# Kernel tuning notes

Hardware: AMD Instinct MI355X
Metric: run time of the kernel (lower is better)

Reference implementation:

```python
import jax, jax.numpy as jnp
import numpy as np

B, S, DIM = 2, 2048, 2048
NH, NKV = 16, 16
HD = 128            # constructor head_dim (full per-head dim, = 2 * self.head_dim)
HHD = HD // 2       # self.head_dim = per-stream dim = 64
ROPE_THETA = 10000.0
LAMBDA_INIT = 0.8 - 0.6 * float(np.exp(-0.3 * 0))  # block_id = 0 -> 0.2
EPS = 1e-5


def make_freq_cis(seq_len, dim, theta):
    # rotation matrices, shape (seq, dim//2, 2, 2): [[cos, -sin], [sin, cos]]
    inv = 1.0 / (theta ** (np.arange(0, dim, 2, dtype=np.float32) / dim))
    ang = np.arange(seq_len, dtype=np.float32)[:, None] * inv[None, :]
    cos, sin = np.cos(ang), np.sin(ang)
    fc = np.stack([np.stack([cos, -sin], -1), np.stack([sin, cos], -1)], -2)
    return jnp.asarray(fc, dtype=jnp.float32)


def setup_inputs() -> dict:
    key = jax.random.key(0)
    ks = jax.random.split(key, 9)
    std = DIM ** -0.5
    return {
        "x": jax.random.normal(ks[0], (B, S, DIM), jnp.float32),
        "freq_cis": make_freq_cis(S, HD, ROPE_THETA),
        "wq": jax.random.normal(ks[1], (NH * HD, DIM), jnp.float32) * std,
        "wk": jax.random.normal(ks[2], (NKV * HD, DIM), jnp.float32) * std,
        "wv": jax.random.normal(ks[3], (NKV * HD, DIM), jnp.float32) * std,
        "wo": jax.random.normal(ks[4], (DIM, NH * HD), jnp.float32) * std,
        "lambda_q1": jax.random.normal(ks[5], (HHD,), jnp.float32) * 0.1,
        "lambda_k1": jax.random.normal(ks[6], (HHD,), jnp.float32) * 0.1,
        "lambda_q2": jax.random.normal(ks[7], (HHD,), jnp.float32) * 0.1,
        "lambda_k2": jax.random.normal(ks[8], (HHD,), jnp.float32) * 0.1,
        "subln_w": jnp.ones((HD,), jnp.float32),
    }


def _rope(t, fc):
    # t: (b, s, h, d); fc: (s, d//2, 2, 2). Pairs (even, odd) rotated by 2x2 matrix.
    b, s, h, d = t.shape
    t2 = t.reshape(b, s, h, d // 2, 1, 2)
    out = (t2 * fc[None, :, None]).sum(-1)  # (b, s, h, d//2, 2)
    return out.reshape(b, s, h, d)


def _causal_attn(q, k, v):
    # q, k: (b, s, h, HHD); v: (b, s, h, HD). Flash-attn default scale = 1/sqrt(q head dim).
    scale = 1.0 / jnp.sqrt(jnp.asarray(q.shape[-1], q.dtype))
    scores = jnp.einsum('bqhd,bkhd->bhqk', q, k) * scale
    s = q.shape[1]
    causal = jnp.tril(jnp.ones((s, s), bool))
    scores = jnp.where(causal, scores, jnp.finfo(scores.dtype).min)
    p = jax.nn.softmax(scores, axis=-1)
    return jnp.einsum('bhqk,bkhd->bqhd', p, v)  # (b, s, h, HD)


def reference(x, freq_cis, wq, wk, wv, wo, lambda_q1, lambda_k1, lambda_q2, lambda_k2, subln_w):
    b, s, _ = x.shape
    xq = (x @ wq.T).reshape(b, s, NH, HD)
    xk = (x @ wk.T).reshape(b, s, NKV, HD)
    xv = (x @ wv.T).reshape(b, s, NKV, HD)
    xq = _rope(xq, freq_cis)
    xk = _rope(xk, freq_cis)
    if NKV != NH:  # GQA: repeat kv heads group-wise
        rep = NH // NKV
        xk = jnp.repeat(xk, rep, axis=2)
        xv = jnp.repeat(xv, rep, axis=2)
    # split each head into two differential streams of size HHD
    xq = xq.reshape(b, s, NH, 2, HHD)
    xk = xk.reshape(b, s, NH, 2, HHD)
    attn1 = _causal_attn(xq[:, :, :, 0], xk[:, :, :, 0], xv)
    attn2 = _causal_attn(xq[:, :, :, 1], xk[:, :, :, 1], xv)
    lam1 = jnp.exp(jnp.sum(lambda_q1 * lambda_k1))
    lam2 = jnp.exp(jnp.sum(lambda_q2 * lambda_k2))
    lam_full = lam1 - lam2 + LAMBDA_INIT
    attn = attn1 - lam_full * attn2              # (b, s, h, HD)
    attn = jnp.transpose(attn, (0, 2, 1, 3))     # faithful to torch .transpose(1, 2)
    ms = jnp.mean(jnp.square(attn), axis=-1, keepdims=True)
    attn = attn * jax.lax.rsqrt(ms + EPS) * subln_w  # RMSNorm(2*HHD)
    attn = attn * (1.0 - LAMBDA_INIT)
    # faithful to original: reshape (b, h, s, HD) row-major into (b, s, h*HD)
    attn = attn.reshape(b, s, NH * HD)
    return attn @ wo.T
```

## Files before the change

### kernel.cpp

```cpp
#include <hip/hip_runtime.h>

typedef unsigned short u16;
typedef unsigned int   u32;
typedef __attribute__((ext_vector_type(8))) short s16x8;
typedef __attribute__((ext_vector_type(4))) float f32x4;

constexpr int Bc = 2, Sc = 2048, DIMc = 2048, NHc = 16, HDc = 128, Tc = Bc * Sc;
constexpr float LAMBDA_INIT_C = 0.2f;

__device__ __forceinline__ u16 f2bf(float f) {
  union { float f; u32 u; } v; v.f = f;
  u32 r = v.u + 0x7fffu + ((v.u >> 16) & 1u);
  return (u16)(r >> 16);
}
__device__ __forceinline__ float bf2f(u16 b) {
  union { u32 u; float f; } v; v.u = ((u32)b) << 16;
  return v.f;
}
__device__ __forceinline__ f32x4 mfma16(s16x8 a, s16x8 b, f32x4 c) {
  return __builtin_amdgcn_mfma_f32_16x16x32_bf16(a, b, c, 0, 0, 0);
}

typedef const __attribute__((address_space(1))) u32 gq32;
typedef __attribute__((address_space(3))) u32 lq32;
__device__ __forceinline__ void cp16(const u16* g, u16* l) {
  __builtin_amdgcn_global_load_lds((gq32*)g, (lq32*)l, 16, 0, 0);
}

__global__ void cvt_all_kernel(const float* __restrict__ x,
                               const float* __restrict__ wq, const float* __restrict__ wk,
                               const float* __restrict__ wv, const float* __restrict__ wo,
                               u16* __restrict__ xb, u16* __restrict__ wb) {
  const int i = blockIdx.x * 256 + threadIdx.x;
  constexpr int NX = Tc * DIMc / 4;
  constexpr int PW = DIMc * DIMc / 4;
  float4 v; uint2* dst;
  if (i < NX) {
    v = ((const float4*)x)[i];
    dst = ((uint2*)xb) + i;
  } else {
    const int j = i - NX;
    const int which = j >> 20;
    const int jj = j & (PW - 1);
    const float* src = which == 0 ? wq : which == 1 ? wk : which == 2 ? wv : wo;
    v = ((const float4*)src)[jj];
    dst = ((uint2*)wb) + j;
  }
  union { u16 u[4]; uint2 p; } o;
  o.u[0] = f2bf(v.x); o.u[1] = f2bf(v.y); o.u[2] = f2bf(v.z); o.u[3] = f2bf(v.w);
  *dst = o.p;
}

__global__ __launch_bounds__(256) void gemm_qkv(const u16* __restrict__ A,
                                                const u16* __restrict__ Wq,
                                                const u16* __restrict__ Wk,
                                                const u16* __restrict__ Wv,
                                                u16* __restrict__ Oq,
                                                u16* __restrict__ Ok,
                                                u16* __restrict__ Ov) {
  constexpr int K = DIMc, N = DIMc;
  __shared__ u16 lA[128 * 32];
  __shared__ u16 lB[128 * 32];
  const int nglob = blockIdx.x * 128;
  const int which = nglob >> 11;
  const u16* Bw = which == 0 ? Wq : which == 1 ? Wk : Wv;
  u16*       Cb = which == 0 ? Oq : which == 1 ? Ok : Ov;
  const int nbase = nglob & (N - 1);
  const int mbase = blockIdx.y * 128;

  const int tid  = threadIdx.x;
  const int lane = tid & 63;
  const int w    = tid >> 6;
  const int wrow = (w >> 1) * 64;
  const int wcol = (w & 1) * 64;
  const int l15  = lane & 15;
  const int quad = lane >> 4;

  f32x4 acc[4][4];
#pragma unroll
  for (int i = 0; i < 4; i++)
#pragma unroll
    for (int j = 0; j < 4; j++) acc[i][j] = (f32x4){0.f, 0.f, 0.f, 0.f};

  const int srow = w * 32 + (lane >> 2);
  const int scol = (lane & 3) * 8;
  const u16* gA = A  + (size_t)(mbase + srow) * K + scol;
  const u16* gB = Bw + (size_t)(nbase + srow) * K + scol;
  u16* sA = lA + srow * 32 + scol;
  u16* sB = lB + srow * 32 + scol;

  for (int kb = 0; kb < K; kb += 32) {
    __syncthreads();
    cp16(gA + kb,                  sA);
    cp16(gA + kb + (size_t)16 * K, sA + 16 * 32);
    cp16(gB + kb,                  sB);
    cp16(gB + kb + (size_t)16 * K, sB + 16 * 32);
    __syncthreads();
    s16x8 af[4], bfr[4];
#pragma unroll
    for (int i = 0; i < 4; i++)
      af[i] = *(const s16x8*)(lA + (wrow + i * 16 + l15) * 32 + quad * 8);
#pragma unroll
    for (int j = 0; j < 4; j++)
      bfr[j] = *(const s16x8*)(lB + (wcol + j * 16 + l15) * 32 + quad * 8);
#pragma unroll
    for (int i = 0; i < 4; i++)
#pragma unroll
      for (int j = 0; j < 4; j++) acc[i][j] = mfma16(af[i], bfr[j], acc[i][j]);
  }

#pragma unroll
  for (int i = 0; i < 4; i++) {
    const int m0 = mbase + wrow + i * 16 + quad * 4;
#pragma unroll
    for (int j = 0; j < 4; j++) {
      const int n0 = nbase + wcol + j * 16 + l15;
#pragma unroll
      for (int r = 0; r < 4; r++) Cb[(size_t)(m0 + r) * N + n0] = f2bf(acc[i][j][r]);
    }
  }
}

__global__ __launch_bounds__(256) void gemm_bt(const u16* __restrict__ A,
                                               const u16* __restrict__ Bw,
                                               float* __restrict__ Cf,
                                               int M, int N, int K) {
  __shared__ u16 lA[128 * 32];
  __shared__ u16 lB[128 * 32];
  const int tid  = threadIdx.x;
  const int lane = tid & 63;
  const int w    = tid >> 6;
  const int mbase = blockIdx.y * 128;
  const int nbase = blockIdx.x * 128;
  const int wrow = (w >> 1) * 64;
  const int wcol = (w & 1) * 64;
  const int l15  = lane & 15;
  const int quad = lane >> 4;

  f32x4 acc[4][4];
#pragma unroll
  for (int i = 0; i < 4; i++)
#pragma unroll
    for (int j = 0; j < 4; j++) acc[i][j] = (f32x4){0.f, 0.f, 0.f, 0.f};

  const int srow = w * 32 + (lane >> 2);
  const int scol = (lane & 3) * 8;
  const u16* gA = A  + (size_t)(mbase + srow) * K + scol;
  const u16* gB = Bw + (size_t)(nbase + srow) * K + scol;
  u16* sA = lA + srow * 32 + scol;
  u16* sB = lB + srow * 32 + scol;

  for (int kb = 0; kb < K; kb += 32) {
    __syncthreads();
    cp16(gA + kb,                  sA);
    cp16(gA + kb + (size_t)16 * K, sA + 16 * 32);
    cp16(gB + kb,                  sB);
    cp16(gB + kb + (size_t)16 * K, sB + 16 * 32);
    __syncthreads();
    s16x8 af[4], bfr[4];
#pragma unroll
    for (int i = 0; i < 4; i++)
      af[i] = *(const s16x8*)(lA + (wrow + i * 16 + l15) * 32 + quad * 8);
#pragma unroll
    for (int j = 0; j < 4; j++)
      bfr[j] = *(const s16x8*)(lB + (wcol + j * 16 + l15) * 32 + quad * 8);
#pragma unroll
    for (int i = 0; i < 4; i++)
#pragma unroll
      for (int j = 0; j < 4; j++) acc[i][j] = mfma16(af[i], bfr[j], acc[i][j]);
  }

#pragma unroll
  for (int i = 0; i < 4; i++) {
    const int m0 = mbase + wrow + i * 16 + quad * 4;
#pragma unroll
    for (int j = 0; j < 4; j++) {
      const int n0 = nbase + wcol + j * 16 + l15;
#pragma unroll
      for (int r = 0; r < 4; r++) Cf[(size_t)(m0 + r) * N + n0] = acc[i][j][r];
    }
  }
}

__global__ void prep_kernel(const u16* __restrict__ qg, const u16* __restrict__ kg,
                            const u16* __restrict__ vg, const float* __restrict__ fc,
                            u16* __restrict__ qr, u16* __restrict__ kr,
                            u16* __restrict__ vt) {
  __shared__ u16 tile[32][33];
  const int bid = blockIdx.x;
  if (bid < 32768) {
    const bool isq = bid < 16384;
    const u16* xg = isq ? qg : kg;
    u16* outp = isq ? qr : kr;
    const float scale = isq ? 0.125f : 1.0f;
    const int idx = (bid & 16383) * 256 + threadIdx.x;
    const int p = idx & 63;
    const int hh = (idx >> 6) & 15;
    const int tt = idx >> 10;
    const int s = tt & (Sc - 1);
    const int bb = tt >> 11;
    const float c  = fc[(size_t)(s * 64 + p) * 4 + 0] * scale;
    const float sn = fc[(size_t)(s * 64 + p) * 4 + 2] * scale;
    const u32 xp = *(const u32*)(xg + (size_t)tt * DIMc + hh * HDc + p * 2);
    const float x0 = bf2f((u16)xp), x1 = bf2f((u16)(xp >> 16));
    const u16 y0 = f2bf(c * x0 - sn * x1);
    const u16 y1 = f2bf(sn * x0 + c * x1);
    *(u32*)(outp + ((size_t)(bb * NHc + hh) * Sc + s) * HDc + p * 2) =
        (u32)y0 | ((u32)y1 << 16);
  } else {
    const int vb = bid - 32768;
    const int bh = vb >> 8;
    const int bb = bh >> 4, hh = bh & 15;
    const int rem = vb & 255;
    const int s0 = (rem & 63) * 32, d0 = (rem >> 6) * 32;
    const int tx = threadIdx.x & 31, ty = threadIdx.x >> 5;
#pragma unroll
    for (int pp = 0; pp < 4; pp++) {
      const int s = s0 + ty + pp * 8;
      tile[ty + pp * 8][tx] = vg[(size_t)(bb * Sc + s) * DIMc + hh * HDc + d0 + tx];
    }
    __syncthreads();
#pragma unroll
    for (int pp = 0; pp < 4; pp++) {
      const int d = d0 + ty + pp * 8;
      vt[((size_t)bh * HDc + d) * Sc + s0 + tx] = tile[tx][ty + pp * 8];
    }
  }
}

__global__ __launch_bounds__(256, 2) void diff_attn_kernel(
    const u16* __restrict__ qr, const u16* __restrict__ kr, const u16* __restrict__ vt,
    const float* __restrict__ lq1, const float* __restrict__ lk1,
    const float* __restrict__ lq2, const float* __restrict__ lk2,
    const float* __restrict__ subw, u16* __restrict__ Y) {
  __shared__ u16 KB[2][8192];
  __shared__ u16 VB[2][8192];

  const int h = blockIdx.y, b = blockIdx.z, jb = blockIdx.x;
  const int bh = b * NHc + h;
  const int tid = threadIdx.x;
  const int w = tid >> 6, lane = tid & 63;
  const int l15 = lane & 15, quad = lane >> 4;

  const u16* krb = kr + (size_t)bh * Sc * HDc;
  const u16* vtb = vt + (size_t)bh * HDc * Sc;

  float lp1 = lq1[lane] * lk1[lane];
  float lp2 = lq2[lane] * lk2[lane];
#pragma unroll
  for (int m = 32; m; m >>= 1) { lp1 += __shfl_xor(lp1, m); lp2 += __shfl_xor(lp2, m); }
  const float lam = __expf(lp1) - __expf(lp2) + LAMBDA_INIT_C;

  float wsub[8];
#pragma unroll
  for (int dn = 0; dn < 8; dn++) wsub[dn] = subw[dn * 16 + l15];

  size_t offK[4], offV[4];
  int dstO[4];
#pragma unroll
  for (int oo = 0; oo < 4; oo++) {
    const int n = w * 256 + oo * 64 + lane;
    const int s = n & 31, dblk = (n >> 5) & 15, sub = n >> 9;
    const int mkey = (s & 3) + ((s >> 2) & 3) * 8 + ((s >> 4) << 2);
    offK[oo] = (size_t)(sub * 32 + mkey) * HDc + dblk * 8;
    offV[oo] = (size_t)(n & 127) * Sc + (sub * 32 + ((n >> 7) & 3) * 8);
    dstO[oo] = n * 8;
  }

  for (int ph = 0; ph < 2; ph++) {
    const int t = ph ? (31 - jb) : jb;
    const int rowbase = t * 64 + w * 16;
    const int nc = t + 1;

    const u16* qp = qr + ((size_t)bh * Sc + rowbase + l15) * HDc + quad * 8;
    s16x8 qa[2][2];
    qa[0][0] = *(const s16x8*)(qp);
    qa[0][1] = *(const s16x8*)(qp + 32);
    qa[1][0] = *(const s16x8*)(qp + 64);
    qa[1][1] = *(const s16x8*)(qp + 96);

    f32x4 o[2][8];
#pragma unroll
    for (int st = 0; st < 2; st++)
#pragma unroll
      for (int dn = 0; dn < 8; dn++) o[st][dn] = (f32x4){0.f, 0.f, 0.f, 0.f};
    float lpart[2] = { 0.f, 0.f };

    __syncthreads();
#pragma unroll
    for (int oo = 0; oo < 4; oo++) cp16(krb + offK[oo], KB[0] + dstO[oo]);
#pragma unroll
    for (int oo = 0; oo < 4; oo++) cp16(vtb + offV[oo], VB[0] + dstO[oo]);

    for (int c = 0; c < nc; c++) {
      __syncthreads();
      if (c + 1 < nc) {
        const int kb1 = (c + 1) * 64;
        u16* Kn = KB[(c + 1) & 1];
        u16* Vn = VB[(c + 1) & 1];
#pragma unroll
        for (int oo = 0; oo < 4; oo++) cp16(krb + (size_t)kb1 * HDc + offK[oo], Kn + dstO[oo]);
#pragma unroll
        for (int oo = 0; oo < 4; oo++) cp16(vtb + offV[oo] + kb1, Vn + dstO[oo]);
      }
      const u16* Kb = KB[c & 1];
      const u16* Vb = VB[c & 1];
      const int kb = c * 64;
      const bool diag = (c == nc - 1);

#pragma unroll
      for (int sub = 0; sub < 2; sub++) {
        if (diag && sub == 1 && w < 2) continue;

        f32x4 sc[2][2];
#pragma unroll
        for (int st = 0; st < 2; st++)
#pragma unroll
          for (int kt = 0; kt < 2; kt++) sc[st][kt] = (f32x4){0.f, 0.f, 0.f, 0.f};
#pragma unroll
        for (int st = 0; st < 2; st++)
#pragma unroll
          for (int kh = 0; kh < 2; kh++) {
            const int base = sub * 512 + (st * 8 + kh * 4 + quad) * 32;
#pragma unroll
            for (int kt = 0; kt < 2; kt++) {
              const s16x8 kf = *(const s16x8*)(Kb + (size_t)(base + kt * 16 + l15) * 8);
              sc[st][kt] = mfma16(kf, qa[st][kh], sc[st][kt]);
            }
          }

        s16x8 pa[2];
#pragma unroll
        for (int st = 0; st < 2; st++) {
          float p[8];
#pragma unroll
          for (int kt = 0; kt < 2; kt++)
#pragma unroll
            for (int r = 0; r < 4; r++) p[kt * 4 + r] = __expf(sc[st][kt][r]);
          if (diag) {
            const int qrow = rowbase + l15;
            const int kb0 = kb + sub * 32 + quad * 8;
#pragma unroll
            for (int j8 = 0; j8 < 8; j8++)
              if (kb0 + j8 > qrow) p[j8] = 0.f;
          }
          float sm = 0.f;
#pragma unroll
          for (int j8 = 0; j8 < 8; j8++) sm += p[j8];
          lpart[st] += sm;
          union { u16 us[8]; s16x8 vv; } pk;
#pragma unroll
          for (int j8 = 0; j8 < 8; j8++) pk.us[j8] = f2bf(p[j8]);
          pa[st] = pk.vv;
        }

#pragma unroll
        for (int dn = 0; dn < 8; dn++) {
          const s16x8 vf =
              *(const s16x8*)(Vb + (size_t)(sub * 512 + quad * 128 + dn * 16 + l15) * 8);
          o[0][dn] = mfma16(pa[0], vf, o[0][dn]);
          o[1][dn] = mfma16(pa[1], vf, o[1][dn]);
        }
      }
    }

    float lL0 = lpart[0], lL1 = lpart[1];
    lL0 += __shfl_xor(lL0, 16); lL0 += __shfl_xor(lL0, 32);
    lL1 += __shfl_xor(lL1, 16); lL1 += __shfl_xor(lL1, 32);
    const float inv1 = 1.f / lL0;
    const float inv2 = lam / lL1;
    float i1C[4], i2C[4];
#pragma unroll
    for (int r = 0; r < 4; r++) {
      i1C[r] = __shfl(inv1, quad * 4 + r, 16);
      i2C[r] = __shfl(inv2, quad * 4 + r, 16);
    }
    float yv[8][4], ss[4] = { 0.f, 0.f, 0.f, 0.f };
#pragma unroll
    for (int dn = 0; dn < 8; dn++)
#pragma unroll
      for (int r = 0; r < 4; r++) {
        const float y = o[0][dn][r] * i1C[r] - o[1][dn][r] * i2C[r];
        yv[dn][r] = y;
        ss[r] += y * y;
      }
#pragma unroll
    for (int r = 0; r < 4; r++) {
#pragma unroll
      for (int mm = 1; mm < 16; mm <<= 1) ss[r] += __shfl_xor(ss[r], mm);
    }
    float scl[4];
#pragma unroll
    for (int r = 0; r < 4; r++) scl[r] = rsqrtf(ss[r] * (1.f / 128.f) + 1e-5f) * 0.8f;

    u16* yrow = Y + ((size_t)(b * Sc + h * 128 + t * 4 + w)) * 2048;
#pragma unroll
    for (int dn = 0; dn < 8; dn++)
#pragma unroll
      for (int r = 0; r < 4; r++)
        yrow[(quad * 4 + r) * 128 + dn * 16 + l15] = f2bf(yv[dn][r] * scl[r] * wsub[dn]);
  }
}

extern "C" void kernel_launch(void* const* d_in, const int* in_sizes, int n_in,
                              void* d_out, int out_size, void* d_ws, size_t ws_size,
                              hipStream_t stream) {
  const float* x    = (const float*)d_in[0];
  const float* fc   = (const float*)d_in[1];
  const float* wq   = (const float*)d_in[2];
  const float* wk   = (const float*)d_in[3];
  const float* wv   = (const float*)d_in[4];
  const float* wo   = (const float*)d_in[5];
  const float* lq1  = (const float*)d_in[6];
  const float* lk1  = (const float*)d_in[7];
  const float* lq2  = (const float*)d_in[8];
  const float* lk2  = (const float*)d_in[9];
  const float* subw = (const float*)d_in[10];
  float* out = (float*)d_out;

  char* ws = (char*)d_ws;
  constexpr size_t SZ_X  = (size_t)Tc * DIMc * 2;
  constexpr size_t SZ_W  = (size_t)DIMc * DIMc * 2;
  constexpr size_t SZ_T  = (size_t)Tc * DIMc * 2;
  u16* xb  = (u16*)(ws);
  u16* wqb = (u16*)(ws + SZ_X);
  u16* wkb = (u16*)(ws + SZ_X + SZ_W);
  u16* wvb = (u16*)(ws + SZ_X + 2 * SZ_W);
  u16* wob = (u16*)(ws + SZ_X + 3 * SZ_W);
  u16* qg  = (u16*)(ws + SZ_X + 4 * SZ_W);
  u16* kg  = (u16*)(ws + SZ_X + 4 * SZ_W + SZ_T);
  u16* vg  = (u16*)(ws + SZ_X + 4 * SZ_W + 2 * SZ_T);
  u16* qr  = (u16*)(ws + SZ_X + 4 * SZ_W + 3 * SZ_T);
  u16* kr  = (u16*)(ws + SZ_X + 4 * SZ_W + 4 * SZ_T);
  u16* vt  = (u16*)(ws + SZ_X + 4 * SZ_W + 5 * SZ_T);
  u16* Y   = (u16*)(ws + SZ_X + 4 * SZ_W + 6 * SZ_T);

  cvt_all_kernel<<<(Tc * DIMc / 4 + 4 * DIMc * DIMc / 4) / 256, 256, 0, stream>>>(
      x, wq, wk, wv, wo, xb, wqb);

  gemm_qkv<<<dim3(48, Tc / 128), 256, 0, stream>>>(xb, wqb, wkb, wvb, qg, kg, vg);

  prep_kernel<<<16384 + 16384 + 8192, 256, 0, stream>>>(qg, kg, vg, fc, qr, kr, vt);

  diff_attn_kernel<<<dim3(16, NHc, Bc), 256, 0, stream>>>(
      qr, kr, vt, lq1, lk1, lq2, lk2, subw, Y);

  gemm_bt<<<dim3(DIMc / 128, Tc / 128), 256, 0, stream>>>(Y, wob, out, Tc, DIMc, DIMc);
}
```

Baseline: 441.5 us.

## Replace GEMMs with double-buffered 8-wave 128x256 pipelined bf16 MFMA kernel

Replaces the simple single-buffered 128x128 GEMMs (QKV projection and output projection) with one templated 512-thread kernel using 128x256 tiles, K-step 64 and double-buffered LDS. Global-to-LDS copies are staged across phases of the MFMA schedule, and an XOR swizzle avoids LDS bank conflicts. It also adds a workgroup-order swizzle for L2 locality and raises MFMA priority with setprio. The QKV GEMM treats the contiguous wq/wk/wv buffers as one 6144-wide weight matrix, which relies on the workspace layout and on qg/kg/vg being contiguous.

```diff
diff --git a/kernel.cpp b/kernel.cpp
--- a/kernel.cpp
+++ b/kernel.cpp
@@ -51,30 +51,56 @@
   *dst = o.p;
 }
 
-__global__ __launch_bounds__(256) void gemm_qkv(const u16* __restrict__ A,
-                                                const u16* __restrict__ Wq,
-                                                const u16* __restrict__ Wk,
-                                                const u16* __restrict__ Wv,
-                                                u16* __restrict__ Oq,
-                                                u16* __restrict__ Ok,
-                                                u16* __restrict__ Ov) {
-  constexpr int K = DIMc, N = DIMc;
-  __shared__ u16 lA[128 * 32];
-  __shared__ u16 lB[128 * 32];
-  const int nglob = blockIdx.x * 128;
-  const int which = nglob >> 11;
-  const u16* Bw = which == 0 ? Wq : which == 1 ? Wk : Wv;
-  u16*       Cb = which == 0 ? Oq : which == 1 ? Ok : Ov;
-  const int nbase = nglob & (N - 1);
-  const int mbase = blockIdx.y * 128;
+template<int MODE>
+__global__ __launch_bounds__(512, 2) void gemm8p(const u16* __restrict__ A,
+                                                 const u16* __restrict__ Bw,
+                                                 u16* __restrict__ Cb,
+                                                 float* __restrict__ Cf,
+                                                 int N) {
+  constexpr int K = 2048, NT = K / 64;
+  constexpr int BUF = 24576;
+  __shared__ __align__(16) u16 L[2 * BUF];
 
   const int tid  = threadIdx.x;
-  const int lane = tid & 63;
-  const int w    = tid >> 6;
-  const int wrow = (w >> 1) * 64;
-  const int wcol = (w & 1) * 64;
-  const int l15  = lane & 15;
-  const int quad = lane >> 4;
+  const int lane = tid & 63, w = tid >> 6;
+  const int wm = w >> 2, wn = w & 3;
+  const int l15 = lane & 15, quad = lane >> 4;
+
+  const int gx   = gridDim.x;
+  const int nwg  = gx * gridDim.y;
+  const int flat = blockIdx.y * gx + blockIdx.x;
+  const int swz  = (flat & 7) * (nwg >> 3) + (flat >> 3);
+  const int nbase = (swz % gx) * 256;
+  const int mbase = (swz / gx) * 128;
+
+  const u16* Ag = A  + (size_t)mbase * K;
+  const u16* Bg = Bw + (size_t)nbase * K;
+
+  u32 soff[2], dlin[2];
+#pragma unroll
+  for (int l = 0; l < 2; l++) {
+    const int n = l * 512 + tid;
+    const int r = n >> 3;
+    const u32 q = (u32)((n & 7) ^ (r & 7));
+    soff[l] = (u32)r * K + q * 8;
+    dlin[l] = (u32)n * 8;
+  }
+
+  auto stA = [&](int kt, int bb) {
+#pragma unroll
+    for (int l = 0; l < 2; l++)
+      cp16(Ag + (size_t)kt * 64 + soff[l], L + bb + dlin[l]);
+  };
+  auto stB = [&](int kt, int h, int bb) {
+#pragma unroll
+    for (int l = 0; l < 2; l++)
+      cp16(Bg + (size_t)h * (128 * K) + (size_t)kt * 64 + soff[l],
+           L + bb + 8192 + h * 8192 + dlin[l]);
+  };
+
+  const int aB  = (wm * 64 + l15) * 64;
+  const int bB  = 8192 + (wn * 64 + l15) * 64;
+  const int xq0 = (quad ^ (l15 & 7)) << 3;
 
   f32x4 acc[4][4];
 #pragma unroll
@@ -82,102 +108,125 @@
 #pragma unroll
     for (int j = 0; j < 4; j++) acc[i][j] = (f32x4){0.f, 0.f, 0.f, 0.f};
 
-  const int srow = w * 32 + (lane >> 2);
-  const int scol = (lane & 3) * 8;
-  const u16* gA = A  + (size_t)(mbase + srow) * K + scol;
-  const u16* gB = Bw + (size_t)(nbase + srow) * K + scol;
-  u16* sA = lA + srow * 32 + scol;
-  u16* sB = lB + srow * 32 + scol;
-
-  for (int kb = 0; kb < K; kb += 32) {
-    __syncthreads();
-    cp16(gA + kb,                  sA);
-    cp16(gA + kb + (size_t)16 * K, sA + 16 * 32);
-    cp16(gB + kb,                  sB);
-    cp16(gB + kb + (size_t)16 * K, sB + 16 * 32);
-    __syncthreads();
-    s16x8 af[4], bfr[4];
-#pragma unroll
-    for (int i = 0; i < 4; i++)
-      af[i] = *(const s16x8*)(lA + (wrow + i * 16 + l15) * 32 + quad * 8);
-#pragma unroll
-    for (int j = 0; j < 4; j++)
-      bfr[j] = *(const s16x8*)(lB + (wcol + j * 16 + l15) * 32 + quad * 8);
-#pragma unroll
-    for (int i = 0; i < 4; i++)
-#pragma unroll
-      for (int j = 0; j < 4; j++) acc[i][j] = mfma16(af[i], bfr[j], acc[i][j]);
-  }
-
-#pragma unroll
-  for (int i = 0; i < 4; i++) {
-    const int m0 = mbase + wrow + i * 16 + quad * 4;
-#pragma unroll
-    for (int j = 0; j < 4; j++) {
-      const int n0 = nbase + wcol + j * 16 + l15;
-#pragma unroll
-      for (int r = 0; r < 4; r++) Cb[(size_t)(m0 + r) * N + n0] = f2bf(acc[i][j][r]);
-    }
-  }
-}
-
-__global__ __launch_bounds__(256) void gemm_bt(const u16* __restrict__ A,
-                                               const u16* __restrict__ Bw,
-                                               float* __restrict__ Cf,
-                                               int M, int N, int K) {
-  __shared__ u16 lA[128 * 32];
-  __shared__ u16 lB[128 * 32];
-  const int tid  = threadIdx.x;
-  const int lane = tid & 63;
-  const int w    = tid >> 6;
-  const int mbase = blockIdx.y * 128;
-  const int nbase = blockIdx.x * 128;
-  const int wrow = (w >> 1) * 64;
-  const int wcol = (w & 1) * 64;
-  const int l15  = lane & 15;
-  const int quad = lane >> 4;
-
-  f32x4 acc[4][4];
-#pragma unroll
-  for (int i = 0; i < 4; i++)
-#pragma unroll
-    for (int j = 0; j < 4; j++) acc[i][j] = (f32x4){0.f, 0.f, 0.f, 0.f};
-
-  const int srow = w * 32 + (lane >> 2);
-  const int scol = (lane & 3) * 8;
-  const u16* gA = A  + (size_t)(mbase + srow) * K + scol;
-  const u16* gB = Bw + (size_t)(nbase + srow) * K + scol;
-  u16* sA = lA + srow * 32 + scol;
-  u16* sB = lB + srow * 32 + scol;
-
-  for (int kb = 0; kb < K; kb += 32) {
-    __syncthreads();
-    cp16(gA + kb,                  sA);
-    cp16(gA + kb + (size_t)16 * K, sA + 16 * 32);
-    cp16(gB + kb,                  sB);
-    cp16(gB + kb + (size_t)16 * K, sB + 16 * 32);
-    __syncthreads();
-    s16x8 af[4], bfr[4];
-#pragma unroll
-    for (int i = 0; i < 4; i++)
-      af[i] = *(const s16x8*)(lA + (wrow + i * 16 + l15) * 32 + quad * 8);
-#pragma unroll
-    for (int j = 0; j < 4; j++)
-      bfr[j] = *(const s16x8*)(lB + (wcol + j * 16 + l15) * 32 + quad * 8);
-#pragma unroll
-    for (int i = 0; i < 4; i++)
-#pragma unroll
-      for (int j = 0; j < 4; j++) acc[i][j] = mfma16(af[i], bfr[j], acc[i][j]);
-  }
-
-#pragma unroll
-  for (int i = 0; i < 4; i++) {
-    const int m0 = mbase + wrow + i * 16 + quad * 4;
-#pragma unroll
-    for (int j = 0; j < 4; j++) {
-      const int n0 = nbase + wcol + j * 16 + l15;
-#pragma unroll
-      for (int r = 0; r < 4; r++) Cf[(size_t)(m0 + r) * N + n0] = acc[i][j][r];
+  stB(0, 0, 0); stB(0, 1, 0); stA(0, 0); stB(1, 0, BUF); stB(1, 1, BUF);
+  asm volatile("s_waitcnt vmcnt(4)" ::: "memory");
+  asm volatile("s_barrier" ::: "memory");
+
+  s16x8 aL[2][2], aH[2][2], b0[2][2], b1[2][2];
+
+  for (int kt = 0; kt < NT; ++kt) {
+    const int cb  = (kt & 1) * BUF;
+    const int nb  = BUF - cb;
+    const int tgA = (kt + 1 < NT) ? kt + 1 : 0;
+    const int tgB = (kt + 2 < NT) ? kt + 2 : 0;
+
+#pragma unroll
+    for (int i = 0; i < 2; i++) {
+      aL[i][0] = *(const s16x8*)(L + cb + aB + i * 1024 + xq0);
+      aL[i][1] = *(const s16x8*)(L + cb + aB + i * 1024 + (xq0 ^ 32));
+    }
+#pragma unroll
+    for (int j = 0; j < 2; j++) {
+      b0[j][0] = *(const s16x8*)(L + cb + bB + j * 1024 + xq0);
+      b0[j][1] = *(const s16x8*)(L + cb + bB + j * 1024 + (xq0 ^ 32));
+    }
+    stA(tgA, nb);
+    asm volatile("s_barrier" ::: "memory");
+    asm volatile("s_waitcnt lgkmcnt(0)" ::: "memory");
+    __builtin_amdgcn_sched_barrier(0);
+    __builtin_amdgcn_s_setprio(1);
+#pragma unroll
+    for (int i = 0; i < 2; i++)
+#pragma unroll
+      for (int j = 0; j < 2; j++) {
+        acc[i][j] = mfma16(aL[i][0], b0[j][0], acc[i][j]);
+        acc[i][j] = mfma16(aL[i][1], b0[j][1], acc[i][j]);
+      }
+    __builtin_amdgcn_s_setprio(0);
+    asm volatile("s_barrier" ::: "memory");
+
+#pragma unroll
+    for (int j = 0; j < 2; j++) {
+      b1[j][0] = *(const s16x8*)(L + cb + bB + (j + 2) * 1024 + xq0);
+      b1[j][1] = *(const s16x8*)(L + cb + bB + (j + 2) * 1024 + (xq0 ^ 32));
+    }
+    asm volatile("s_barrier" ::: "memory");
+    asm volatile("s_waitcnt lgkmcnt(0)" ::: "memory");
+    __builtin_amdgcn_sched_barrier(0);
+    __builtin_amdgcn_s_setprio(1);
+#pragma unroll
+    for (int i = 0; i < 2; i++)
+#pragma unroll
+      for (int j = 0; j < 2; j++) {
+        acc[i][j + 2] = mfma16(aL[i][0], b1[j][0], acc[i][j + 2]);
+        acc[i][j + 2] = mfma16(aL[i][1], b1[j][1], acc[i][j + 2]);
+      }
+    __builtin_amdgcn_s_setprio(0);
+    asm volatile("s_barrier" ::: "memory");
+
+#pragma unroll
+    for (int i = 0; i < 2; i++) {
+      aH[i][0] = *(const s16x8*)(L + cb + aB + (i + 2) * 1024 + xq0);
+      aH[i][1] = *(const s16x8*)(L + cb + aB + (i + 2) * 1024 + (xq0 ^ 32));
+    }
+    stB(tgB, 0, cb);
+    asm volatile("s_barrier" ::: "memory");
+    asm volatile("s_waitcnt lgkmcnt(0)" ::: "memory");
+    __builtin_amdgcn_sched_barrier(0);
+    __builtin_amdgcn_s_setprio(1);
+#pragma unroll
+    for (int i = 0; i < 2; i++)
+#pragma unroll
+      for (int j = 0; j < 2; j++) {
+        acc[i + 2][j + 2] = mfma16(aH[i][0], b1[j][0], acc[i + 2][j + 2]);
+        acc[i + 2][j + 2] = mfma16(aH[i][1], b1[j][1], acc[i + 2][j + 2]);
+      }
+    __builtin_amdgcn_s_setprio(0);
+    asm volatile("s_barrier" ::: "memory");
+
+    stB(tgB, 1, cb);
+    asm volatile("s_waitcnt vmcnt(4)" ::: "memory");
+    asm volatile("s_barrier" ::: "memory");
+    __builtin_amdgcn_sched_barrier(0);
+    __builtin_amdgcn_s_setprio(1);
+#pragma unroll
+    for (int i = 0; i < 2; i++)
+#pragma unroll
+      for (int j = 0; j < 2; j++) {
+        acc[i + 2][j] = mfma16(aH[i][0], b0[j][0], acc[i + 2][j]);
+        acc[i + 2][j] = mfma16(aH[i][1], b0[j][1], acc[i + 2][j]);
+      }
+    __builtin_amdgcn_s_setprio(0);
+    asm volatile("s_barrier" ::: "memory");
+  }
+  asm volatile("s_waitcnt vmcnt(0)" ::: "memory");
+
+  if (MODE == 0) {
+    const int which = nbase >> 11;
+    const int ncol  = nbase & 2047;
+    u16* Ob = Cb + (size_t)which * ((size_t)Tc * DIMc);
+#pragma unroll
+    for (int i = 0; i < 4; i++) {
+      const int m0 = mbase + wm * 64 + i * 16 + quad * 4;
+#pragma unroll
+      for (int j = 0; j < 4; j++) {
+        const int n0 = ncol + wn * 64 + j * 16 + l15;
+#pragma unroll
+        for (int r = 0; r < 4; r++)
+          Ob[(size_t)(m0 + r) * 2048 + n0] = f2bf(acc[i][j][r]);
+      }
+    }
+  } else {
+#pragma unroll
+    for (int i = 0; i < 4; i++) {
+      const int m0 = mbase + wm * 64 + i * 16 + quad * 4;
+#pragma unroll
+      for (int j = 0; j < 4; j++) {
+        const int n0 = nbase + wn * 64 + j * 16 + l15;
+#pragma unroll
+        for (int r = 0; r < 4; r++)
+          Cf[(size_t)(m0 + r) * N + n0] = acc[i][j][r];
+      }
     }
   }
 }
@@ -424,8 +473,6 @@
   constexpr size_t SZ_T  = (size_t)Tc * DIMc * 2;
   u16* xb  = (u16*)(ws);
   u16* wqb = (u16*)(ws + SZ_X);
-  u16* wkb = (u16*)(ws + SZ_X + SZ_W);
-  u16* wvb = (u16*)(ws + SZ_X + 2 * SZ_W);
   u16* wob = (u16*)(ws + SZ_X + 3 * SZ_W);
   u16* qg  = (u16*)(ws + SZ_X + 4 * SZ_W);
   u16* kg  = (u16*)(ws + SZ_X + 4 * SZ_W + SZ_T);
@@ -438,12 +485,14 @@
   cvt_all_kernel<<<(Tc * DIMc / 4 + 4 * DIMc * DIMc / 4) / 256, 256, 0, stream>>>(
       x, wq, wk, wv, wo, xb, wqb);
 
-  gemm_qkv<<<dim3(48, Tc / 128), 256, 0, stream>>>(xb, wqb, wkb, wvb, qg, kg, vg);
+  gemm8p<0><<<dim3(DIMc * 3 / 256, Tc / 128), 512, 0, stream>>>(
+      xb, wqb, qg, nullptr, 3 * DIMc);
 
   prep_kernel<<<16384 + 16384 + 8192, 256, 0, stream>>>(qg, kg, vg, fc, qr, kr, vt);
 
   diff_attn_kernel<<<dim3(16, NHc, Bc), 256, 0, stream>>>(
       qr, kr, vt, lq1, lk1, lq2, lk2, subw, Y);
 
-  gemm_bt<<<dim3(DIMc / 128, Tc / 128), 256, 0, stream>>>(Y, wob, out, Tc, DIMc, DIMc);
-}
+  gemm8p<1><<<dim3(DIMc / 256, Tc / 128), 512, 0, stream>>>(
+      Y, wob, nullptr, out, DIMc);
+}
```

Measured after the change: 412.7 us. 1.07x faster.
